# Kernel tuning notes

Measured on AMD Instinct MI355X. Metric: run time of the kernel, lower is better.

The kernel has to match this reference:

```python
import jax, jax.numpy as jnp
import numpy as np

CUTOFF = 5.0
LOG2 = float(np.log(2.0))

def ssp(x):
    # shifted softplus: softplus(x) - log(2)
    return jax.nn.softplus(x) - LOG2

def setup_inputs() -> dict:
    key = jax.random.key(0)
    ks = jax.random.split(key, 12)
    Nb, Na, Nnbh = 8, 1024, 64
    A, F, S = 128, 128, 50
    x = jax.random.normal(ks[0], (Nb, Na, A), dtype=jnp.float32)
    r_ij = jax.random.uniform(ks[1], (Nb, Na, Nnbh), dtype=jnp.float32) * 8.0  # some beyond cutoff=5
    neighbors = jax.random.randint(ks[2], (Nb, Na, Nnbh), 0, Na)
    neighbor_mask = (jax.random.uniform(ks[3], (Nb, Na, Nnbh)) > 0.1).astype(jnp.float32)
    f_ij = jax.random.normal(ks[4], (Nb, Na, Nnbh, S), dtype=jnp.float32)
    sc = lambda n: 1.0 / np.sqrt(n)
    W_in2f = jax.random.normal(ks[5], (F, A), dtype=jnp.float32) * sc(A)
    W_f1 = jax.random.normal(ks[6], (F, S), dtype=jnp.float32) * sc(S)
    b_f1 = jnp.zeros((F,), jnp.float32)
    W_f2 = jax.random.normal(ks[7], (F, F), dtype=jnp.float32) * sc(F)
    b_f2 = jnp.zeros((F,), jnp.float32)
    W_f2out = jax.random.normal(ks[8], (A, F), dtype=jnp.float32) * sc(F)
    b_f2out = jnp.zeros((A,), jnp.float32)
    W_dense = jax.random.normal(ks[9], (A, A), dtype=jnp.float32) * sc(A)
    b_dense = jnp.zeros((A,), jnp.float32)
    return {"x": x, "r_ij": r_ij, "neighbors": neighbors, "neighbor_mask": neighbor_mask,
            "f_ij": f_ij, "W_in2f": W_in2f, "W_f1": W_f1, "b_f1": b_f1, "W_f2": W_f2,
            "b_f2": b_f2, "W_f2out": W_f2out, "b_f2out": b_f2out, "W_dense": W_dense,
            "b_dense": b_dense}

def reference(x, r_ij, neighbors, neighbor_mask, f_ij, W_in2f, W_f1, b_f1, W_f2, b_f2,
              W_f2out, b_f2out, W_dense, b_dense):
    # filter network: Dense(S->F, ssp) -> Dense(F->F)
    W = ssp(jnp.einsum('bans,fs->banf', f_ij, W_f1) + b_f1)
    W = jnp.einsum('bang,fg->banf', W, W_f2) + b_f2          # [Nb,Na,Nnbh,F]
    # hard cutoff
    C = (r_ij <= CUTOFF).astype(W.dtype)                      # [Nb,Na,Nnbh]
    W = W * C[..., None]
    # in2f (no bias)
    y = jnp.einsum('bai,fi->baf', x, W_in2f)                  # [Nb,Na,F]
    # gather neighbor features along atom axis
    yg = jax.vmap(lambda yb, nb: yb[nb])(y, neighbors)        # [Nb,Na,Nnbh,F]
    # masked sum over neighbor axis (Aggregate, mean=False)
    v = jnp.sum(yg * W * neighbor_mask[..., None], axis=2)    # [Nb,Na,F]
    # f2out: Dense(F->A) with ssp, then dense: Dense(A->A)
    v = ssp(jnp.einsum('baf,af->ba' + 'f'[0:0] + 'a'[0:0], v, W_f2out).reshape(v.shape[:2] + (W_f2out.shape[0],)) if False else ssp(v @ W_f2out.T + b_f2out))
    out = v @ W_dense.T + b_dense                             # [Nb,Na,A]
    return out
```

## Files before the change

### kernel.cpp

```cpp
#include <hip/hip_runtime.h>
#include <math.h>


#define RCUT  5.0f
#define LOG2F_ 0.69314718055994530942f
#define LOG2E_ 1.44269504088896340736f

typedef __bf16 bf16x8_t __attribute__((ext_vector_type(8)));
typedef float  f32x4_t  __attribute__((ext_vector_type(4)));

static __device__ __forceinline__ float sspf(float x) {
    float e  = exp2f(-LOG2E_ * fabsf(x));
    float lg = log2f(1.0f + e);
    return fmaf(lg, LOG2F_, fmaxf(x, 0.0f) - LOG2F_);
}
static __device__ __forceinline__ unsigned pack2h(__bf16 a, __bf16 b) {
    union { __bf16 h[2]; unsigned u; } un; un.h[0] = a; un.h[1] = b; return un.u;
}
static __device__ __forceinline__ unsigned pack2f(float a, float b) {
    return pack2h((__bf16)a, (__bf16)b);
}

__global__ __launch_bounds__(256) void prep_kernel(
    const float* __restrict__ W1, const float* __restrict__ W2,
    const float* __restrict__ Wb,
    const float* __restrict__ Wc,
    const float* __restrict__ Wf,
    unsigned* __restrict__ prep)
{
    int i = blockIdx.x * 256 + threadIdx.x;
    if (i < 4096) {
        int sw = i >> 10, ft = (i >> 9) & 1, kh = (i >> 8) & 1;
        int sl = (i >> 2) & 63, j = i & 3;
        int sq = sl >> 4, sm = sl & 15;
        int f = 32 * sw + 16 * ft + sm;
        int c = kh * 16 + 4 * sq + j;
        int k0 = 2 * c, k1 = 2 * c + 1;
        float a = (k0 < 50) ? W1[f * 50 + k0] : 0.0f;
        float b = (k1 < 50) ? W1[f * 50 + k1] : 0.0f;
        prep[i] = pack2f(a, b);
    } else if (i < 12288) {
        int s = i - 4096;
        int sw = s >> 11, ft = (s >> 10) & 1, kq = (s >> 8) & 3;
        int sl = (s >> 2) & 63, j = s & 3;
        int sq = sl >> 4, sm = sl & 15;
        int f = 32 * sw + 16 * ft + sm;
        int c = 16 * kq + 4 * sq + j;
        float2 wv = ((const float2*)W2)[f * 64 + c];
        prep[i] = pack2f(wv.x, wv.y);
    } else {
        int s = i - 12288;
        int L = s >> 14;
        int r = s & 16383;
        int hl = r >> 13;
        int e = r & 8191;
        int sw = e >> 11, ft = (e >> 10) & 1, kq = (e >> 8) & 3;
        int sl = (e >> 2) & 63, j = e & 3;
        int sq = sl >> 4, sm = sl & 15;
        int f = 32 * sw + 16 * ft + sm;
        int c = 16 * kq + 4 * sq + j;
        const float* src = (L == 0) ? Wb : (L == 1) ? Wc : Wf;
        float2 wv = ((const float2*)src)[f * 64 + c];
        if (hl == 0) {
            prep[i] = pack2h((__bf16)wv.x, (__bf16)wv.y);
        } else {
            __bf16 h0 = (__bf16)wv.x, h1 = (__bf16)wv.y;
            prep[i] = pack2f(wv.x - (float)h0, wv.y - (float)h1);
        }
    }
}

__global__ __launch_bounds__(256, 4) void k1_kernel(
    const float* __restrict__ x,
    const unsigned* __restrict__ Wh, const unsigned* __restrict__ Wl,
    float* __restrict__ yout)
{
    __shared__ __bf16 Ah[16 * 136];
    __shared__ __bf16 Al[16 * 136];

    const int t = threadIdx.x;
    const int atom0 = (blockIdx.x >> 1) * 16;
    const int fh = blockIdx.x & 1;
    const int w = t >> 6, l = t & 63, m = l & 15, q = l >> 4;

    {
        const float4* A4 = (const float4*)(x + (size_t)atom0 * 128);
        unsigned* AhU = (unsigned*)Ah;
        unsigned* AlU = (unsigned*)Al;
        #pragma unroll
        for (int r = 0; r < 2; ++r) {
            int lin4 = r * 256 + t;
            int a = lin4 >> 5, k4 = lin4 & 31;
            float4 xv = A4[lin4];
            __bf16 h0=(__bf16)xv.x, h1=(__bf16)xv.y, h2=(__bf16)xv.z, h3=(__bf16)xv.w;
            int idx = a * 68 + 2 * k4;
            AhU[idx]     = pack2h(h0, h1);
            AhU[idx + 1] = pack2h(h2, h3);
            AlU[idx]     = pack2f(xv.x - (float)h0, xv.y - (float)h1);
            AlU[idx + 1] = pack2f(xv.z - (float)h2, xv.w - (float)h3);
        }
    }
    __syncthreads();

    const int ftile = fh * 4 + w;
    const int f = 16 * ftile + m;
    f32x4_t acc = {0.f, 0.f, 0.f, 0.f};
    #pragma unroll
    for (int kk = 0; kk < 4; ++kk) {
        int off = m * 136 + 32 * kk + 8 * q;
        bf16x8_t ah = *(const bf16x8_t*)&Ah[off];
        bf16x8_t al = *(const bf16x8_t*)&Al[off];
        int wo = (ftile * 4 + kk) * 256 + l * 4;
        bf16x8_t wh = *(const bf16x8_t*)(Wh + wo);
        bf16x8_t wl = *(const bf16x8_t*)(Wl + wo);
        acc = __builtin_amdgcn_mfma_f32_16x16x32_bf16(ah, wh, acc, 0, 0, 0);
        acc = __builtin_amdgcn_mfma_f32_16x16x32_bf16(ah, wl, acc, 0, 0, 0);
        acc = __builtin_amdgcn_mfma_f32_16x16x32_bf16(al, wh, acc, 0, 0, 0);
    }
    #pragma unroll
    for (int r = 0; r < 4; ++r)
        yout[(size_t)(atom0 + 4 * q + r) * 128 + f] = acc[r];
}

__global__ __launch_bounds__(256, 4) void interaction_kernel(
    const float* __restrict__ rij, const int* __restrict__ nbrs,
    const float* __restrict__ mask, const float* __restrict__ fij,
    const float* __restrict__ b1, const float* __restrict__ b2,
    const unsigned* __restrict__ W1S,
    const unsigned* __restrict__ W2S,
    const float* __restrict__ y, float* __restrict__ v)
{
    __shared__ __bf16 Hh[64 * 136];
    __shared__ __bf16 Hl[64 * 136];
    __shared__ float  cb[64];
    __shared__ int    nb[64];

    const int t  = threadIdx.x;
    const int a  = blockIdx.x;
    const int bi = a >> 10;
    const int p0 = a * 64;
    const int w = t >> 6, l = t & 63, m = l & 15, q = l >> 4;
    const int f0 = 32 * w + m;
    const int f1 = f0 + 16;

    bf16x8_t w2f0[4], w2f1[4];
    #pragma unroll
    for (int kq = 0; kq < 4; ++kq) {
        w2f0[kq] = *(const bf16x8_t*)(W2S + ((w * 2 + 0) * 4 + kq) * 256 + l * 4);
        w2f1[kq] = *(const bf16x8_t*)(W2S + ((w * 2 + 1) * 4 + kq) * 256 + l * 4);
    }

    if (t < 64) {
        float r = rij[p0 + t];
        cb[t] = (r <= RCUT) ? mask[p0 + t] : 0.0f;
        nb[t] = (bi << 10) + nbrs[p0 + t];
    }

    {
        const float* frow = fij + (size_t)(p0 + 16 * w + m) * 50;
        float kv[16];
        #pragma unroll
        for (int j2 = 0; j2 < 4; ++j2) {
            float2 xv = *(const float2*)(frow + 8 * q + 2 * j2);
            kv[2 * j2] = xv.x; kv[2 * j2 + 1] = xv.y;
        }
        #pragma unroll
        for (int j2 = 0; j2 < 4; ++j2) {
            int k = 32 + 8 * q + 2 * j2;
            float2 xv = make_float2(0.f, 0.f);
            if (k < 50) xv = *(const float2*)(frow + k);
            kv[8 + 2 * j2] = xv.x; kv[9 + 2 * j2] = xv.y;
        }
        union { __bf16 h[16]; bf16x8_t v8[2]; } uh, ul;
        #pragma unroll
        for (int k = 0; k < 16; ++k) {
            __bf16 hi = (__bf16)kv[k];
            uh.h[k] = hi;
            ul.h[k] = (__bf16)(kv[k] - (float)hi);
        }
        #pragma unroll 2
        for (int ftile = 0; ftile < 8; ++ftile) {
            float bb = b1[16 * ftile + m];
            f32x4_t acch = {bb, bb, bb, bb};
            f32x4_t accl = {0.f, 0.f, 0.f, 0.f};
            bf16x8_t w0 = *(const bf16x8_t*)(W1S + (ftile * 2 + 0) * 256 + l * 4);
            bf16x8_t w1 = *(const bf16x8_t*)(W1S + (ftile * 2 + 1) * 256 + l * 4);
            acch = __builtin_amdgcn_mfma_f32_16x16x32_bf16(uh.v8[0], w0, acch, 0, 0, 0);
            accl = __builtin_amdgcn_mfma_f32_16x16x32_bf16(ul.v8[0], w0, accl, 0, 0, 0);
            acch = __builtin_amdgcn_mfma_f32_16x16x32_bf16(uh.v8[1], w1, acch, 0, 0, 0);
            accl = __builtin_amdgcn_mfma_f32_16x16x32_bf16(ul.v8[1], w1, accl, 0, 0, 0);
            #pragma unroll
            for (int r = 0; r < 4; ++r) {
                int n = 16 * w + 4 * q + r;
                float hv = sspf(acch[r] + accl[r]);
                __bf16 hh = (__bf16)hv;
                Hh[n * 136 + 16 * ftile + m] = hh;
                Hl[n * 136 + 16 * ftile + m] = (__bf16)(hv - (float)hh);
            }
        }
    }
    __syncthreads();

    float yv0[16], yv1[16];
    #pragma unroll
    for (int i = 0; i < 16; ++i) {
        int n = 16 * (i >> 2) + 4 * q + (i & 3);
        const float* yrow = y + (size_t)nb[n] * 128;
        yv0[i] = yrow[f0];
        yv1[i] = yrow[f1];
    }

    const float bb2_0 = b2[f0], bb2_1 = b2[f1];
    float pv0 = 0.0f, pv1 = 0.0f;
    #pragma unroll
    for (int mt = 0; mt < 4; ++mt) {
        f32x4_t a0h = {bb2_0, bb2_0, bb2_0, bb2_0};
        f32x4_t a0l = {0.f, 0.f, 0.f, 0.f};
        f32x4_t a1h = {bb2_1, bb2_1, bb2_1, bb2_1};
        f32x4_t a1l = {0.f, 0.f, 0.f, 0.f};
        #pragma unroll
        for (int kq = 0; kq < 4; ++kq) {
            int hoff = (16 * mt + m) * 136 + 32 * kq + 8 * q;
            bf16x8_t hh = *(const bf16x8_t*)&Hh[hoff];
            bf16x8_t hl = *(const bf16x8_t*)&Hl[hoff];
            a0h = __builtin_amdgcn_mfma_f32_16x16x32_bf16(hh, w2f0[kq], a0h, 0, 0, 0);
            a0l = __builtin_amdgcn_mfma_f32_16x16x32_bf16(hl, w2f0[kq], a0l, 0, 0, 0);
            a1h = __builtin_amdgcn_mfma_f32_16x16x32_bf16(hh, w2f1[kq], a1h, 0, 0, 0);
            a1l = __builtin_amdgcn_mfma_f32_16x16x32_bf16(hl, w2f1[kq], a1l, 0, 0, 0);
        }
        #pragma unroll
        for (int r = 0; r < 4; ++r) {
            int n = 16 * mt + 4 * q + r;
            float cn = cb[n];
            float s0 = a0h[r] + a0l[r];
            float s1 = a1h[r] + a1l[r];
            pv0 = fmaf(cn * yv0[mt * 4 + r], s0, pv0);
            pv1 = fmaf(cn * yv1[mt * 4 + r], s1, pv1);
        }
    }
    pv0 += __shfl_xor(pv0, 16);
    pv0 += __shfl_xor(pv0, 32);
    pv1 += __shfl_xor(pv1, 16);
    pv1 += __shfl_xor(pv1, 32);
    if (l < 16) {
        v[(size_t)a * 128 + f0] = pv0;
        v[(size_t)a * 128 + f1] = pv1;
    }
}

__global__ __launch_bounds__(256, 4) void mgemm2_kernel(
    const float* A,
    const unsigned* __restrict__ W1h, const unsigned* __restrict__ W1l,
    const float* __restrict__ bias1, int nssp1,
    const unsigned* __restrict__ W2h, const unsigned* __restrict__ W2l,
    const float* __restrict__ bias2, int nssp2,
    float* C)
{
    extern __shared__ float smf[];
    __bf16* Ah = (__bf16*)smf;
    __bf16* Al = (__bf16*)(smf + 1088);
    unsigned* AhU = (unsigned*)Ah;
    unsigned* AlU = (unsigned*)Al;

    const int t = threadIdx.x;
    const int atom0 = blockIdx.x * 16;
    const int w = t >> 6, l = t & 63, m = l & 15, q = l >> 4;

    {
        const float4* A4 = (const float4*)(A + (size_t)atom0 * 128);
        #pragma unroll
        for (int r = 0; r < 2; ++r) {
            int lin4 = r * 256 + t;
            int a = lin4 >> 5, k4 = lin4 & 31;
            float4 xv = A4[lin4];
            __bf16 h0=(__bf16)xv.x, h1=(__bf16)xv.y, h2=(__bf16)xv.z, h3=(__bf16)xv.w;
            int idx = a * 68 + 2 * k4;
            AhU[idx]     = pack2h(h0, h1);
            AhU[idx + 1] = pack2h(h2, h3);
            AlU[idx]     = pack2f(xv.x - (float)h0, xv.y - (float)h1);
            AlU[idx + 1] = pack2f(xv.z - (float)h2, xv.w - (float)h3);
        }
    }
    __syncthreads();

    bf16x8_t ah[4], al[4];
    #pragma unroll
    for (int kk = 0; kk < 4; ++kk) {
        int off = m * 136 + 32 * kk + 8 * q;
        ah[kk] = *(const bf16x8_t*)&Ah[off];
        al[kk] = *(const bf16x8_t*)&Al[off];
    }
    f32x4_t acc[2];
    int fidx[2];
    #pragma unroll
    for (int ft = 0; ft < 2; ++ft) {
        fidx[ft] = 16 * (2 * w + ft) + m;
        float b = bias1 ? bias1[fidx[ft]] : 0.0f;
        acc[ft] = (f32x4_t){b, b, b, b};
    }
    #pragma unroll
    for (int ft = 0; ft < 2; ++ft) {
        #pragma unroll
        for (int kk = 0; kk < 4; ++kk) {
            int wo = ((2 * w + ft) * 4 + kk) * 256 + l * 4;
            bf16x8_t wh = *(const bf16x8_t*)(W1h + wo);
            bf16x8_t wl = *(const bf16x8_t*)(W1l + wo);
            acc[ft] = __builtin_amdgcn_mfma_f32_16x16x32_bf16(ah[kk], wh, acc[ft], 0, 0, 0);
            acc[ft] = __builtin_amdgcn_mfma_f32_16x16x32_bf16(ah[kk], wl, acc[ft], 0, 0, 0);
            acc[ft] = __builtin_amdgcn_mfma_f32_16x16x32_bf16(al[kk], wh, acc[ft], 0, 0, 0);
        }
    }
    #pragma unroll
    for (int ft = 0; ft < 2; ++ft)
        #pragma unroll
        for (int r = 0; r < 4; ++r) {
            float o = acc[ft][r];
            if (nssp1 >= 1) o = sspf(o);
            if (nssp1 >= 2) o = sspf(o);
            acc[ft][r] = o;
        }

    __syncthreads();
    #pragma unroll
    for (int ft = 0; ft < 2; ++ft)
        #pragma unroll
        for (int r = 0; r < 4; ++r) {
            float o = acc[ft][r];
            __bf16 hh = (__bf16)o;
            Ah[(4 * q + r) * 136 + fidx[ft]] = hh;
            Al[(4 * q + r) * 136 + fidx[ft]] = (__bf16)(o - (float)hh);
        }
    __syncthreads();

    #pragma unroll
    for (int kk = 0; kk < 4; ++kk) {
        int off = m * 136 + 32 * kk + 8 * q;
        ah[kk] = *(const bf16x8_t*)&Ah[off];
        al[kk] = *(const bf16x8_t*)&Al[off];
    }
    #pragma unroll
    for (int ft = 0; ft < 2; ++ft) {
        float b = bias2 ? bias2[fidx[ft]] : 0.0f;
        acc[ft] = (f32x4_t){b, b, b, b};
    }
    #pragma unroll
    for (int ft = 0; ft < 2; ++ft) {
        #pragma unroll
        for (int kk = 0; kk < 4; ++kk) {
            int wo = ((2 * w + ft) * 4 + kk) * 256 + l * 4;
            bf16x8_t wh = *(const bf16x8_t*)(W2h + wo);
            bf16x8_t wl = *(const bf16x8_t*)(W2l + wo);
            acc[ft] = __builtin_amdgcn_mfma_f32_16x16x32_bf16(ah[kk], wh, acc[ft], 0, 0, 0);
            acc[ft] = __builtin_amdgcn_mfma_f32_16x16x32_bf16(ah[kk], wl, acc[ft], 0, 0, 0);
            acc[ft] = __builtin_amdgcn_mfma_f32_16x16x32_bf16(al[kk], wh, acc[ft], 0, 0, 0);
        }
    }
    #pragma unroll
    for (int ft = 0; ft < 2; ++ft)
        #pragma unroll
        for (int r = 0; r < 4; ++r) {
            float o = acc[ft][r];
            if (nssp2 >= 1) o = sspf(o);
            if (nssp2 >= 2) o = sspf(o);
            C[(size_t)(atom0 + 4 * q + r) * 128 + fidx[ft]] = o;
        }
}

extern "C" void kernel_launch(void* const* d_in, const int* in_sizes, int n_in,
                              void* d_out, int out_size, void* d_ws, size_t ws_size,
                              hipStream_t stream) {
    const float* x        = (const float*)d_in[0];
    const float* rij      = (const float*)d_in[1];
    const int*   nbrs     = (const int*)  d_in[2];
    const float* mask     = (const float*)d_in[3];
    const float* fij      = (const float*)d_in[4];
    const float* W_in2f   = (const float*)d_in[5];
    const float* W_f1     = (const float*)d_in[6];
    const float* b_f1     = (const float*)d_in[7];
    const float* W_f2     = (const float*)d_in[8];
    const float* b_f2     = (const float*)d_in[9];
    const float* W_f2out  = (const float*)d_in[10];
    const float* b_f2out  = (const float*)d_in[11];
    const float* W_dense  = (const float*)d_in[12];
    const float* b_dense  = (const float*)d_in[13];
    float* out = (float*)d_out;

    float*    y    = (float*)d_ws;
    unsigned* prep = (unsigned*)((char*)d_ws + (4u << 20));
    const unsigned* W1S    = prep;
    const unsigned* W2S    = prep + 4096;
    const unsigned* f2o_h  = prep + 12288, *f2o_l  = prep + 20480;
    const unsigned* den_h  = prep + 28672, *den_l  = prep + 36864;
    const unsigned* in2f_h = prep + 45056, *in2f_l = prep + 53248;

    const int MG2_LDS = 2176 * 4;

    prep_kernel<<<240, 256, 0, stream>>>(W_f1, W_f2, W_f2out, W_dense, W_in2f, prep);
    k1_kernel<<<1024, 256, 0, stream>>>(x, in2f_h, in2f_l, y);
    interaction_kernel<<<8192, 256, 0, stream>>>(
        rij, nbrs, mask, fij, b_f1, b_f2, W1S, W2S, y, out);
    mgemm2_kernel<<<512, 256, MG2_LDS, stream>>>(
        out, f2o_h, f2o_l, b_f2out, 2, den_h, den_l, b_dense, 0, out);
}
```

Baseline: 255.3 us.

## Split interaction kernel into two half-neighbor passes to halve LDS and raise occupancy

The interaction kernel now processes the 64 neighbors in two passes of 32, so the hidden-activation LDS buffers shrink by half and launch bounds rise to 6 blocks per SM. W2 fragments are reloaded from global inside the loop instead of being held in registers. The per-neighbor gathered y values are premultiplied by the cutoff/mask and held only for the current half. This reduces register and LDS pressure to allow more resident waves, at the cost of extra barriers, repeated W2 loads, and a serialized two-phase loop.

```diff
diff --git a/kernel.cpp b/kernel.cpp
--- a/kernel.cpp
+++ b/kernel.cpp
@@ -122,7 +122,7 @@
         yout[(size_t)(atom0 + 4 * q + r) * 128 + f] = acc[r];
 }
 
-__global__ __launch_bounds__(256, 4) void interaction_kernel(
+__global__ __launch_bounds__(256, 6) void interaction_kernel(
     const float* __restrict__ rij, const int* __restrict__ nbrs,
     const float* __restrict__ mask, const float* __restrict__ fij,
     const float* __restrict__ b1, const float* __restrict__ b2,
@@ -130,8 +130,8 @@
     const unsigned* __restrict__ W2S,
     const float* __restrict__ y, float* __restrict__ v)
 {
-    __shared__ __bf16 Hh[64 * 136];
-    __shared__ __bf16 Hl[64 * 136];
+    __shared__ __bf16 Hh[32 * 136];
+    __shared__ __bf16 Hl[32 * 136];
     __shared__ float  cb[64];
     __shared__ int    nb[64];
 
@@ -140,15 +140,10 @@
     const int bi = a >> 10;
     const int p0 = a * 64;
     const int w = t >> 6, l = t & 63, m = l & 15, q = l >> 4;
+    const int rb  = w & 1;
+    const int fh2 = w >> 1;
     const int f0 = 32 * w + m;
     const int f1 = f0 + 16;
-
-    bf16x8_t w2f0[4], w2f1[4];
-    #pragma unroll
-    for (int kq = 0; kq < 4; ++kq) {
-        w2f0[kq] = *(const bf16x8_t*)(W2S + ((w * 2 + 0) * 4 + kq) * 256 + l * 4);
-        w2f1[kq] = *(const bf16x8_t*)(W2S + ((w * 2 + 1) * 4 + kq) * 256 + l * 4);
-    }
 
     if (t < 64) {
         float r = rij[p0 + t];
@@ -156,88 +151,95 @@
         nb[t] = (bi << 10) + nbrs[p0 + t];
     }
 
-    {
-        const float* frow = fij + (size_t)(p0 + 16 * w + m) * 50;
-        float kv[16];
-        #pragma unroll
-        for (int j2 = 0; j2 < 4; ++j2) {
-            float2 xv = *(const float2*)(frow + 8 * q + 2 * j2);
-            kv[2 * j2] = xv.x; kv[2 * j2 + 1] = xv.y;
-        }
-        #pragma unroll
-        for (int j2 = 0; j2 < 4; ++j2) {
-            int k = 32 + 8 * q + 2 * j2;
-            float2 xv = make_float2(0.f, 0.f);
-            if (k < 50) xv = *(const float2*)(frow + k);
-            kv[8 + 2 * j2] = xv.x; kv[9 + 2 * j2] = xv.y;
-        }
-        union { __bf16 h[16]; bf16x8_t v8[2]; } uh, ul;
-        #pragma unroll
-        for (int k = 0; k < 16; ++k) {
-            __bf16 hi = (__bf16)kv[k];
-            uh.h[k] = hi;
-            ul.h[k] = (__bf16)(kv[k] - (float)hi);
-        }
-        #pragma unroll 2
-        for (int ftile = 0; ftile < 8; ++ftile) {
-            float bb = b1[16 * ftile + m];
-            f32x4_t acch = {bb, bb, bb, bb};
-            f32x4_t accl = {0.f, 0.f, 0.f, 0.f};
-            bf16x8_t w0 = *(const bf16x8_t*)(W1S + (ftile * 2 + 0) * 256 + l * 4);
-            bf16x8_t w1 = *(const bf16x8_t*)(W1S + (ftile * 2 + 1) * 256 + l * 4);
-            acch = __builtin_amdgcn_mfma_f32_16x16x32_bf16(uh.v8[0], w0, acch, 0, 0, 0);
-            accl = __builtin_amdgcn_mfma_f32_16x16x32_bf16(ul.v8[0], w0, accl, 0, 0, 0);
-            acch = __builtin_amdgcn_mfma_f32_16x16x32_bf16(uh.v8[1], w1, acch, 0, 0, 0);
-            accl = __builtin_amdgcn_mfma_f32_16x16x32_bf16(ul.v8[1], w1, accl, 0, 0, 0);
-            #pragma unroll
-            for (int r = 0; r < 4; ++r) {
-                int n = 16 * w + 4 * q + r;
-                float hv = sspf(acch[r] + accl[r]);
-                __bf16 hh = (__bf16)hv;
-                Hh[n * 136 + 16 * ftile + m] = hh;
-                Hl[n * 136 + 16 * ftile + m] = (__bf16)(hv - (float)hh);
-            }
-        }
-    }
-    __syncthreads();
-
-    float yv0[16], yv1[16];
-    #pragma unroll
-    for (int i = 0; i < 16; ++i) {
-        int n = 16 * (i >> 2) + 4 * q + (i & 3);
-        const float* yrow = y + (size_t)nb[n] * 128;
-        yv0[i] = yrow[f0];
-        yv1[i] = yrow[f1];
-    }
-
     const float bb2_0 = b2[f0], bb2_1 = b2[f1];
     float pv0 = 0.0f, pv1 = 0.0f;
-    #pragma unroll
-    for (int mt = 0; mt < 4; ++mt) {
-        f32x4_t a0h = {bb2_0, bb2_0, bb2_0, bb2_0};
-        f32x4_t a0l = {0.f, 0.f, 0.f, 0.f};
-        f32x4_t a1h = {bb2_1, bb2_1, bb2_1, bb2_1};
-        f32x4_t a1l = {0.f, 0.f, 0.f, 0.f};
-        #pragma unroll
-        for (int kq = 0; kq < 4; ++kq) {
-            int hoff = (16 * mt + m) * 136 + 32 * kq + 8 * q;
-            bf16x8_t hh = *(const bf16x8_t*)&Hh[hoff];
-            bf16x8_t hl = *(const bf16x8_t*)&Hl[hoff];
-            a0h = __builtin_amdgcn_mfma_f32_16x16x32_bf16(hh, w2f0[kq], a0h, 0, 0, 0);
-            a0l = __builtin_amdgcn_mfma_f32_16x16x32_bf16(hl, w2f0[kq], a0l, 0, 0, 0);
-            a1h = __builtin_amdgcn_mfma_f32_16x16x32_bf16(hh, w2f1[kq], a1h, 0, 0, 0);
-            a1l = __builtin_amdgcn_mfma_f32_16x16x32_bf16(hl, w2f1[kq], a1l, 0, 0, 0);
-        }
-        #pragma unroll
-        for (int r = 0; r < 4; ++r) {
-            int n = 16 * mt + 4 * q + r;
+
+    #pragma unroll 1
+    for (int h = 0; h < 2; ++h) {
+        {
+            const float* frow = fij + (size_t)(p0 + 32 * h + 16 * rb + m) * 50;
+            float kv[16];
+            #pragma unroll
+            for (int j2 = 0; j2 < 4; ++j2) {
+                float2 xv = *(const float2*)(frow + 8 * q + 2 * j2);
+                kv[2 * j2] = xv.x; kv[2 * j2 + 1] = xv.y;
+            }
+            #pragma unroll
+            for (int j2 = 0; j2 < 4; ++j2) {
+                int k = 32 + 8 * q + 2 * j2;
+                float2 xv = make_float2(0.f, 0.f);
+                if (k < 50) xv = *(const float2*)(frow + k);
+                kv[8 + 2 * j2] = xv.x; kv[9 + 2 * j2] = xv.y;
+            }
+            union { __bf16 hh[16]; bf16x8_t v8[2]; } uh, ul;
+            #pragma unroll
+            for (int k = 0; k < 16; ++k) {
+                __bf16 hi = (__bf16)kv[k];
+                uh.hh[k] = hi;
+                ul.hh[k] = (__bf16)(kv[k] - (float)hi);
+            }
+            #pragma unroll
+            for (int ft4 = 0; ft4 < 4; ++ft4) {
+                int ftile = 4 * fh2 + ft4;
+                float bb = b1[16 * ftile + m];
+                f32x4_t acch = {bb, bb, bb, bb};
+                f32x4_t accl = {0.f, 0.f, 0.f, 0.f};
+                bf16x8_t w0 = *(const bf16x8_t*)(W1S + (ftile * 2 + 0) * 256 + l * 4);
+                bf16x8_t w1 = *(const bf16x8_t*)(W1S + (ftile * 2 + 1) * 256 + l * 4);
+                acch = __builtin_amdgcn_mfma_f32_16x16x32_bf16(uh.v8[0], w0, acch, 0, 0, 0);
+                accl = __builtin_amdgcn_mfma_f32_16x16x32_bf16(ul.v8[0], w0, accl, 0, 0, 0);
+                acch = __builtin_amdgcn_mfma_f32_16x16x32_bf16(uh.v8[1], w1, acch, 0, 0, 0);
+                accl = __builtin_amdgcn_mfma_f32_16x16x32_bf16(ul.v8[1], w1, accl, 0, 0, 0);
+                #pragma unroll
+                for (int r = 0; r < 4; ++r) {
+                    int n = 16 * rb + 4 * q + r;
+                    float hv = sspf(acch[r] + accl[r]);
+                    __bf16 hh = (__bf16)hv;
+                    Hh[n * 136 + 16 * ftile + m] = hh;
+                    Hl[n * 136 + 16 * ftile + m] = (__bf16)(hv - (float)hh);
+                }
+            }
+        }
+        __syncthreads();
+
+        float cy0[8], cy1[8];
+        #pragma unroll
+        for (int i = 0; i < 8; ++i) {
+            int n = 32 * h + 16 * (i >> 2) + 4 * q + (i & 3);
+            const float* yrow = y + (size_t)nb[n] * 128;
             float cn = cb[n];
-            float s0 = a0h[r] + a0l[r];
-            float s1 = a1h[r] + a1l[r];
-            pv0 = fmaf(cn * yv0[mt * 4 + r], s0, pv0);
-            pv1 = fmaf(cn * yv1[mt * 4 + r], s1, pv1);
-        }
-    }
+            cy0[i] = cn * yrow[f0];
+            cy1[i] = cn * yrow[f1];
+        }
+        #pragma unroll
+        for (int mtl = 0; mtl < 2; ++mtl) {
+            f32x4_t a0h = {bb2_0, bb2_0, bb2_0, bb2_0};
+            f32x4_t a0l = {0.f, 0.f, 0.f, 0.f};
+            f32x4_t a1h = {bb2_1, bb2_1, bb2_1, bb2_1};
+            f32x4_t a1l = {0.f, 0.f, 0.f, 0.f};
+            #pragma unroll
+            for (int kq = 0; kq < 4; ++kq) {
+                int hoff = (16 * mtl + m) * 136 + 32 * kq + 8 * q;
+                bf16x8_t hh = *(const bf16x8_t*)&Hh[hoff];
+                bf16x8_t hl = *(const bf16x8_t*)&Hl[hoff];
+                bf16x8_t w20 = *(const bf16x8_t*)(W2S + ((w * 2 + 0) * 4 + kq) * 256 + l * 4);
+                bf16x8_t w21 = *(const bf16x8_t*)(W2S + ((w * 2 + 1) * 4 + kq) * 256 + l * 4);
+                a0h = __builtin_amdgcn_mfma_f32_16x16x32_bf16(hh, w20, a0h, 0, 0, 0);
+                a0l = __builtin_amdgcn_mfma_f32_16x16x32_bf16(hl, w20, a0l, 0, 0, 0);
+                a1h = __builtin_amdgcn_mfma_f32_16x16x32_bf16(hh, w21, a1h, 0, 0, 0);
+                a1l = __builtin_amdgcn_mfma_f32_16x16x32_bf16(hl, w21, a1l, 0, 0, 0);
+            }
+            #pragma unroll
+            for (int r = 0; r < 4; ++r) {
+                float s0 = a0h[r] + a0l[r];
+                float s1 = a1h[r] + a1l[r];
+                pv0 = fmaf(cy0[mtl * 4 + r], s0, pv0);
+                pv1 = fmaf(cy1[mtl * 4 + r], s1, pv1);
+            }
+        }
+        if (h == 0) __syncthreads();
+    }
+
     pv0 += __shfl_xor(pv0, 16);
     pv0 += __shfl_xor(pv0, 32);
     pv1 += __shfl_xor(pv1, 16);
```

New measurement: 607.3 us. +137.9%, slower.

## Split filter-network hidden layer into two K-halves to halve shared memory

Applied to the files above, without the earlier changes.

The interaction kernel now computes the first filter layer in two passes of 64 hidden features each. Each pass is consumed by a partial second-layer GEMM that accumulates into the running sums, so the Hh/Hl shared buffers shrink from 64x136 to 64x72 bf16 each. W2 fragments are loaded per pass instead of being held in registers for the whole kernel, and the cutoff*y products are precomputed once. The aim is lower LDS and register pressure so more blocks can be resident per CU. The cost is two extra __syncthreads and reloading W2 slices per pass.

```diff
diff --git a/kernel.cpp b/kernel.cpp
--- a/kernel.cpp
+++ b/kernel.cpp
@@ -122,6 +122,84 @@
         yout[(size_t)(atom0 + 4 * q + r) * 128 + f] = acc[r];
 }
 
+template<int PASS>
+static __device__ __forceinline__ void k2A(
+    const unsigned* __restrict__ W1S, const float* __restrict__ b1,
+    const bf16x8_t (&uhv)[2], const bf16x8_t (&ulv)[2],
+    int w, int m, int q, int l,
+    __bf16* __restrict__ Hh, __bf16* __restrict__ Hl)
+{
+    #pragma unroll
+    for (int ft4 = 0; ft4 < 4; ++ft4) {
+        const int ftile = 4 * PASS + ft4;
+        float bb = b1[16 * ftile + m];
+        f32x4_t acch = {bb, bb, bb, bb};
+        f32x4_t accl = {0.f, 0.f, 0.f, 0.f};
+        bf16x8_t w0 = *(const bf16x8_t*)(W1S + (ftile * 2 + 0) * 256 + l * 4);
+        bf16x8_t w1 = *(const bf16x8_t*)(W1S + (ftile * 2 + 1) * 256 + l * 4);
+        acch = __builtin_amdgcn_mfma_f32_16x16x32_bf16(uhv[0], w0, acch, 0, 0, 0);
+        accl = __builtin_amdgcn_mfma_f32_16x16x32_bf16(ulv[0], w0, accl, 0, 0, 0);
+        acch = __builtin_amdgcn_mfma_f32_16x16x32_bf16(uhv[1], w1, acch, 0, 0, 0);
+        accl = __builtin_amdgcn_mfma_f32_16x16x32_bf16(ulv[1], w1, accl, 0, 0, 0);
+        #pragma unroll
+        for (int r = 0; r < 4; ++r) {
+            int n = 16 * w + 4 * q + r;
+            float hv = sspf(acch[r] + accl[r]);
+            __bf16 hh = (__bf16)hv;
+            Hh[n * 72 + 16 * ft4 + m] = hh;
+            Hl[n * 72 + 16 * ft4 + m] = (__bf16)(hv - (float)hh);
+        }
+    }
+}
+
+template<int PASS>
+static __device__ __forceinline__ void k2B(
+    const unsigned* __restrict__ W2S,
+    const __bf16* __restrict__ Hh, const __bf16* __restrict__ Hl,
+    const float (&cy0)[16], const float (&cy1)[16],
+    int m, int q, int w, int l,
+    float bb2_0, float bb2_1,
+    float& pv0, float& pv1)
+{
+    bf16x8_t w2a[2], w2b[2];
+    #pragma unroll
+    for (int kqL = 0; kqL < 2; ++kqL) {
+        const int kq = 2 * PASS + kqL;
+        w2a[kqL] = *(const bf16x8_t*)(W2S + ((w * 2 + 0) * 4 + kq) * 256 + l * 4);
+        w2b[kqL] = *(const bf16x8_t*)(W2S + ((w * 2 + 1) * 4 + kq) * 256 + l * 4);
+    }
+    #pragma unroll
+    for (int mt = 0; mt < 4; ++mt) {
+        f32x4_t a0h, a1h;
+        if (PASS == 0) {
+            a0h = (f32x4_t){bb2_0, bb2_0, bb2_0, bb2_0};
+            a1h = (f32x4_t){bb2_1, bb2_1, bb2_1, bb2_1};
+        } else {
+            a0h = (f32x4_t){0.f, 0.f, 0.f, 0.f};
+            a1h = (f32x4_t){0.f, 0.f, 0.f, 0.f};
+        }
+        f32x4_t a0l = {0.f, 0.f, 0.f, 0.f};
+        f32x4_t a1l = {0.f, 0.f, 0.f, 0.f};
+        #pragma unroll
+        for (int kqL = 0; kqL < 2; ++kqL) {
+            int hoff = (16 * mt + m) * 72 + 32 * kqL + 8 * q;
+            bf16x8_t hh = *(const bf16x8_t*)&Hh[hoff];
+            bf16x8_t hl = *(const bf16x8_t*)&Hl[hoff];
+            a0h = __builtin_amdgcn_mfma_f32_16x16x32_bf16(hh, w2a[kqL], a0h, 0, 0, 0);
+            a0l = __builtin_amdgcn_mfma_f32_16x16x32_bf16(hl, w2a[kqL], a0l, 0, 0, 0);
+            a1h = __builtin_amdgcn_mfma_f32_16x16x32_bf16(hh, w2b[kqL], a1h, 0, 0, 0);
+            a1l = __builtin_amdgcn_mfma_f32_16x16x32_bf16(hl, w2b[kqL], a1l, 0, 0, 0);
+        }
+        #pragma unroll
+        for (int r = 0; r < 4; ++r) {
+            float s0 = a0h[r] + a0l[r];
+            float s1 = a1h[r] + a1l[r];
+            pv0 = fmaf(cy0[mt * 4 + r], s0, pv0);
+            pv1 = fmaf(cy1[mt * 4 + r], s1, pv1);
+        }
+    }
+}
+
 __global__ __launch_bounds__(256, 4) void interaction_kernel(
     const float* __restrict__ rij, const int* __restrict__ nbrs,
     const float* __restrict__ mask, const float* __restrict__ fij,
@@ -130,8 +208,8 @@
     const unsigned* __restrict__ W2S,
     const float* __restrict__ y, float* __restrict__ v)
 {
-    __shared__ __bf16 Hh[64 * 136];
-    __shared__ __bf16 Hl[64 * 136];
+    __shared__ __bf16 Hh[64 * 72];
+    __shared__ __bf16 Hl[64 * 72];
     __shared__ float  cb[64];
     __shared__ int    nb[64];
 
@@ -143,19 +221,13 @@
     const int f0 = 32 * w + m;
     const int f1 = f0 + 16;
 
-    bf16x8_t w2f0[4], w2f1[4];
-    #pragma unroll
-    for (int kq = 0; kq < 4; ++kq) {
-        w2f0[kq] = *(const bf16x8_t*)(W2S + ((w * 2 + 0) * 4 + kq) * 256 + l * 4);
-        w2f1[kq] = *(const bf16x8_t*)(W2S + ((w * 2 + 1) * 4 + kq) * 256 + l * 4);
-    }
-
     if (t < 64) {
         float r = rij[p0 + t];
         cb[t] = (r <= RCUT) ? mask[p0 + t] : 0.0f;
         nb[t] = (bi << 10) + nbrs[p0 + t];
     }
 
+    bf16x8_t uhv[2], ulv[2];
     {
         const float* frow = fij + (size_t)(p0 + 16 * w + m) * 50;
         float kv[16];
@@ -171,73 +243,39 @@
             if (k < 50) xv = *(const float2*)(frow + k);
             kv[8 + 2 * j2] = xv.x; kv[9 + 2 * j2] = xv.y;
         }
-        union { __bf16 h[16]; bf16x8_t v8[2]; } uh, ul;
+        union { __bf16 e[16]; bf16x8_t v8[2]; } uh, ul;
         #pragma unroll
         for (int k = 0; k < 16; ++k) {
             __bf16 hi = (__bf16)kv[k];
-            uh.h[k] = hi;
-            ul.h[k] = (__bf16)(kv[k] - (float)hi);
-        }
-        #pragma unroll 2
-        for (int ftile = 0; ftile < 8; ++ftile) {
-            float bb = b1[16 * ftile + m];
-            f32x4_t acch = {bb, bb, bb, bb};
-            f32x4_t accl = {0.f, 0.f, 0.f, 0.f};
-            bf16x8_t w0 = *(const bf16x8_t*)(W1S + (ftile * 2 + 0) * 256 + l * 4);
-            bf16x8_t w1 = *(const bf16x8_t*)(W1S + (ftile * 2 + 1) * 256 + l * 4);
-            acch = __builtin_amdgcn_mfma_f32_16x16x32_bf16(uh.v8[0], w0, acch, 0, 0, 0);
-            accl = __builtin_amdgcn_mfma_f32_16x16x32_bf16(ul.v8[0], w0, accl, 0, 0, 0);
-            acch = __builtin_amdgcn_mfma_f32_16x16x32_bf16(uh.v8[1], w1, acch, 0, 0, 0);
-            accl = __builtin_amdgcn_mfma_f32_16x16x32_bf16(ul.v8[1], w1, accl, 0, 0, 0);
-            #pragma unroll
-            for (int r = 0; r < 4; ++r) {
-                int n = 16 * w + 4 * q + r;
-                float hv = sspf(acch[r] + accl[r]);
-                __bf16 hh = (__bf16)hv;
-                Hh[n * 136 + 16 * ftile + m] = hh;
-                Hl[n * 136 + 16 * ftile + m] = (__bf16)(hv - (float)hh);
-            }
-        }
-    }
-    __syncthreads();
-
-    float yv0[16], yv1[16];
+            uh.e[k] = hi;
+            ul.e[k] = (__bf16)(kv[k] - (float)hi);
+        }
+        uhv[0] = uh.v8[0]; uhv[1] = uh.v8[1];
+        ulv[0] = ul.v8[0]; ulv[1] = ul.v8[1];
+    }
+
+    k2A<0>(W1S, b1, uhv, ulv, w, m, q, l, Hh, Hl);
+    __syncthreads();
+
+    float cy0[16], cy1[16];
     #pragma unroll
     for (int i = 0; i < 16; ++i) {
         int n = 16 * (i >> 2) + 4 * q + (i & 3);
         const float* yrow = y + (size_t)nb[n] * 128;
-        yv0[i] = yrow[f0];
-        yv1[i] = yrow[f1];
+        float cn = cb[n];
+        cy0[i] = cn * yrow[f0];
+        cy1[i] = cn * yrow[f1];
     }
 
     const float bb2_0 = b2[f0], bb2_1 = b2[f1];
     float pv0 = 0.0f, pv1 = 0.0f;
-    #pragma unroll
-    for (int mt = 0; mt < 4; ++mt) {
-        f32x4_t a0h = {bb2_0, bb2_0, bb2_0, bb2_0};
-        f32x4_t a0l = {0.f, 0.f, 0.f, 0.f};
-        f32x4_t a1h = {bb2_1, bb2_1, bb2_1, bb2_1};
-        f32x4_t a1l = {0.f, 0.f, 0.f, 0.f};
-        #pragma unroll
-        for (int kq = 0; kq < 4; ++kq) {
-            int hoff = (16 * mt + m) * 136 + 32 * kq + 8 * q;
-            bf16x8_t hh = *(const bf16x8_t*)&Hh[hoff];
-            bf16x8_t hl = *(const bf16x8_t*)&Hl[hoff];
-            a0h = __builtin_amdgcn_mfma_f32_16x16x32_bf16(hh, w2f0[kq], a0h, 0, 0, 0);
-            a0l = __builtin_amdgcn_mfma_f32_16x16x32_bf16(hl, w2f0[kq], a0l, 0, 0, 0);
-            a1h = __builtin_amdgcn_mfma_f32_16x16x32_bf16(hh, w2f1[kq], a1h, 0, 0, 0);
-            a1l = __builtin_amdgcn_mfma_f32_16x16x32_bf16(hl, w2f1[kq], a1l, 0, 0, 0);
-        }
-        #pragma unroll
-        for (int r = 0; r < 4; ++r) {
-            int n = 16 * mt + 4 * q + r;
-            float cn = cb[n];
-            float s0 = a0h[r] + a0l[r];
-            float s1 = a1h[r] + a1l[r];
-            pv0 = fmaf(cn * yv0[mt * 4 + r], s0, pv0);
-            pv1 = fmaf(cn * yv1[mt * 4 + r], s1, pv1);
-        }
-    }
+    k2B<0>(W2S, Hh, Hl, cy0, cy1, m, q, w, l, bb2_0, bb2_1, pv0, pv1);
+    __syncthreads();
+
+    k2A<1>(W1S, b1, uhv, ulv, w, m, q, l, Hh, Hl);
+    __syncthreads();
+    k2B<1>(W2S, Hh, Hl, cy0, cy1, m, q, w, l, bb2_0, bb2_1, pv0, pv1);
+
     pv0 += __shfl_xor(pv0, 16);
     pv0 += __shfl_xor(pv0, 32);
     pv1 += __shfl_xor(pv1, 16);
```

Result: slower. 285.5 us (+11.8%).
